# Kernel optimization log

Measured on AMD Instinct MI355X. Metric: run time of the kernel, lower is better.

Reference implementation:

```python
import jax, jax.numpy as jnp
import numpy as np

B, L, R, E, H = 256, 196, 1024, 1024, 512  # batch, regions, rnn_size, input_encoding, att_hid


def _lstm_cell(x, h, c, Wih, Whh, bih, bhh):
    # PyTorch LSTMCell gate order: i, f, g, o
    gates = x @ Wih.T + bih + h @ Whh.T + bhh  # [B, 4R]
    i, f, g, o = jnp.split(gates, 4, axis=1)
    i, f, o = jax.nn.sigmoid(i), jax.nn.sigmoid(f), jax.nn.sigmoid(o)
    g = jnp.tanh(g)
    c_new = f * c + i * g
    h_new = o * jnp.tanh(c_new)
    return h_new, c_new


def _attention(h, att_feats, p_att, mask, Wh, bh, Wa, ba):
    att_h = h @ Wh.T + bh                       # [B, H]
    dot = jnp.tanh(p_att + att_h[:, None, :])   # [B, L, H]
    scores = jnp.einsum('blh,h->bl', dot, Wa) + ba  # [B, L]
    w = jax.nn.softmax(scores, axis=1)
    w = w * mask
    w = w / (jnp.sum(w, axis=1, keepdims=True) + 1e-10)
    return jnp.einsum('bl,bld->bd', w, att_feats)  # [B, R]


def setup_inputs() -> dict:
    key = jax.random.key(0)
    ks = jax.random.split(key, 32)
    s = 0.05
    inp = {
        'xt': jax.random.normal(ks[0], (B, E), jnp.float32),
        'fc_feats': jax.random.normal(ks[1], (B, 3 * R), jnp.float32),
        'att_feats': jax.random.normal(ks[2], (B, L, R), jnp.float32),
        'p_att_feats': jax.random.normal(ks[3], (B, L, H), jnp.float32),
        'att_masks': jnp.ones((B, L), jnp.float32),
        'att_feats1': jax.random.normal(ks[4], (B, L, R), jnp.float32),
        'p_att_feats1': jax.random.normal(ks[5], (B, L, H), jnp.float32),
        'att_masks1': jnp.ones((B, L), jnp.float32),
        'state_h': jax.random.normal(ks[6], (3, B, R), jnp.float32),
        'state_c': jax.random.normal(ks[7], (3, B, R), jnp.float32),
        # att_lstm0 / att_lstm: input dim E + 2R; lang_lstm: 3R
        'Wih0': jax.random.normal(ks[8], (4 * R, E + 2 * R), jnp.float32) * s,
        'Whh0': jax.random.normal(ks[9], (4 * R, R), jnp.float32) * s,
        'bih0': jnp.zeros((4 * R,), jnp.float32),
        'bhh0': jnp.zeros((4 * R,), jnp.float32),
        'Wih1': jax.random.normal(ks[10], (4 * R, E + 2 * R), jnp.float32) * s,
        'Whh1': jax.random.normal(ks[11], (4 * R, R), jnp.float32) * s,
        'bih1': jnp.zeros((4 * R,), jnp.float32),
        'bhh1': jnp.zeros((4 * R,), jnp.float32),
        'WihL': jax.random.normal(ks[12], (4 * R, 3 * R), jnp.float32) * s,
        'WhhL': jax.random.normal(ks[13], (4 * R, R), jnp.float32) * s,
        'bihL': jnp.zeros((4 * R,), jnp.float32),
        'bhhL': jnp.zeros((4 * R,), jnp.float32),
        # attention0 / attention / attention1 params (h2att + alpha_net)
        'a0_Wh': jax.random.normal(ks[14], (H, R), jnp.float32) * s,
        'a0_bh': jnp.zeros((H,), jnp.float32),
        'a0_Wa': jax.random.normal(ks[15], (H,), jnp.float32) * s,
        'a0_ba': jnp.zeros((), jnp.float32),
        'a_Wh': jax.random.normal(ks[16], (H, R), jnp.float32) * s,
        'a_bh': jnp.zeros((H,), jnp.float32),
        'a_Wa': jax.random.normal(ks[17], (H,), jnp.float32) * s,
        'a_ba': jnp.zeros((), jnp.float32),
        'a1_Wh': jax.random.normal(ks[18], (H, R), jnp.float32) * s,
        'a1_bh': jnp.zeros((H,), jnp.float32),
        'a1_Wa': jax.random.normal(ks[19], (H,), jnp.float32) * s,
        'a1_ba': jnp.zeros((), jnp.float32),
    }
    return inp


def reference(xt, fc_feats, att_feats, p_att_feats, att_masks,
              att_feats1, p_att_feats1, att_masks1, state_h, state_c,
              Wih0, Whh0, bih0, bhh0, Wih1, Whh1, bih1, bhh1,
              WihL, WhhL, bihL, bhhL,
              a0_Wh, a0_bh, a0_Wa, a0_ba,
              a_Wh, a_bh, a_Wa, a_ba,
              a1_Wh, a1_bh, a1_Wa, a1_ba):
    prev_h = state_h[-1]                       # h_lang from previous step
    fc_ori = fc_feats[:, :R]                   # only the first slice is used

    # layer 0: att_lstm0 + attention0 over (att_feats1, p_att_feats1)
    x0 = jnp.concatenate([prev_h, fc_ori, xt], axis=1)
    h_att0, c_att0 = _lstm_cell(x0, state_h[0], state_c[0], Wih0, Whh0, bih0, bhh0)
    att0 = _attention(h_att0, att_feats1, p_att_feats1, att_masks1, a0_Wh, a0_bh, a0_Wa, a0_ba)

    # layer 1: att_lstm + two attentions
    x1 = jnp.concatenate([prev_h, att0, xt], axis=1)
    h_att, c_att = _lstm_cell(x1, state_h[1], state_c[1], Wih1, Whh1, bih1, bhh1)
    att = _attention(h_att, att_feats, p_att_feats, att_masks, a_Wh, a_bh, a_Wa, a_ba)
    att1 = _attention(h_att, att_feats1, p_att_feats1, att_masks1, a1_Wh, a1_bh, a1_Wa, a1_ba)

    # layer 2: lang_lstm
    xL = jnp.concatenate([att, att1, h_att], axis=1)
    h_lang, c_lang = _lstm_cell(xL, state_h[2], state_c[2], WihL, WhhL, bihL, bhhL)

    output = h_lang  # dropout is identity in eval mode
    new_h = jnp.stack([h_att0, h_att, h_lang])
    new_c = jnp.stack([c_att0, c_att, c_lang])
    return output, new_h, new_c
```

## Files before the change

kernel.cpp:

```cpp
#include <hip/hip_runtime.h>
#include <math.h>

#define B_   256
#define L_   196
#define R_   1024
#define E_   1024
#define H_   512
#define G4R  4096
#define DIN  3072

typedef short v4s __attribute__((ext_vector_type(4)));
typedef short v8s __attribute__((ext_vector_type(8)));
typedef float v4f __attribute__((ext_vector_type(4)));

__device__ __forceinline__ float sigmoidf_(float x) {
    return 1.0f / (1.0f + __expf(-x));
}
__device__ __forceinline__ float tanhf_(float x) {
    float ax = fabsf(x);
    float t  = __expf(-2.0f * ax);
    float r  = (1.0f - t) / (1.0f + t);
    return copysignf(r, x);
}

__device__ __forceinline__ void split2(float x, short& hi, short& lo) {
    unsigned u = __float_as_uint(x);
    hi = (short)(u >> 16);
    float r = x - __uint_as_float(u & 0xFFFF0000u);
    lo = (short)(__float_as_uint(r) >> 16);
}

template<int MT, int NT>
__global__ __launch_bounds__(256) void gemm_mfma(
    const float* __restrict__ A1, const float* __restrict__ W1, int K1, int lda1,
    const float* __restrict__ A2, const float* __restrict__ W2, int K2, int lda2,
    const float* __restrict__ bias1, const float* __restrict__ bias2,
    float* __restrict__ C, int N)
{
    constexpr int FM  = MT / 32;
    constexpr int FN  = NT / 32;
    constexpr int ACH = (MT * 32) / 1024;
    constexpr int WCH = (NT * 32) / 1024;

    __shared__ alignas(16) short Ahi[MT][40];
    __shared__ alignas(16) short Alo[MT][40];
    __shared__ alignas(16) short Whi[NT][40];
    __shared__ alignas(16) short Wlo[NT][40];

    const int t     = threadIdx.x;
    const int lane  = t & 63;
    const int wave  = t >> 6;
    const int waveM = wave & 1;
    const int waveN = wave >> 1;
    const int l16   = lane & 15;
    const int quad  = lane >> 4;
    const int mBase = blockIdx.x * MT;
    const int nBase = blockIdx.y * NT;

    v4f acc[FM][FN] = {};

    for (int seg = 0; seg < 2; ++seg) {
        const int K = seg ? K2 : K1;
        if (K == 0) continue;
        const float* Ag  = seg ? A2 : A1;
        const float* Wg  = seg ? W2 : W1;
        const int    lda = seg ? lda2 : lda1;

        for (int k0 = 0; k0 < K; k0 += 32) {
            __syncthreads();
            #pragma unroll
            for (int c = 0; c < ACH; ++c) {
                int flat = t * 4 + c * 1024;
                int row  = flat >> 5, k = flat & 31;
                float4 v = *(const float4*)(Ag + (size_t)(mBase + row) * lda + k0 + k);
                short h0, h1, h2, h3, l0, l1, l2, l3;
                split2(v.x, h0, l0); split2(v.y, h1, l1);
                split2(v.z, h2, l2); split2(v.w, h3, l3);
                v4s hv = { h0, h1, h2, h3 };
                v4s lv = { l0, l1, l2, l3 };
                *(v4s*)&Ahi[row][k] = hv;
                *(v4s*)&Alo[row][k] = lv;
            }
            #pragma unroll
            for (int c = 0; c < WCH; ++c) {
                int flat = t * 4 + c * 1024;
                int row  = flat >> 5, k = flat & 31;
                float4 v = *(const float4*)(Wg + (size_t)(nBase + row) * K + k0 + k);
                short h0, h1, h2, h3, l0, l1, l2, l3;
                split2(v.x, h0, l0); split2(v.y, h1, l1);
                split2(v.z, h2, l2); split2(v.w, h3, l3);
                v4s hv = { h0, h1, h2, h3 };
                v4s lv = { l0, l1, l2, l3 };
                *(v4s*)&Whi[row][k] = hv;
                *(v4s*)&Wlo[row][k] = lv;
            }
            __syncthreads();

            v8s ah[FM], al[FM], wh[FN], wl[FN];
            #pragma unroll
            for (int fi = 0; fi < FM; ++fi) {
                int r = waveM * (MT / 2) + fi * 16 + l16;
                ah[fi] = *(const v8s*)&Ahi[r][quad * 8];
                al[fi] = *(const v8s*)&Alo[r][quad * 8];
            }
            #pragma unroll
            for (int fj = 0; fj < FN; ++fj) {
                int r = waveN * (NT / 2) + fj * 16 + l16;
                wh[fj] = *(const v8s*)&Whi[r][quad * 8];
                wl[fj] = *(const v8s*)&Wlo[r][quad * 8];
            }

            #pragma unroll
            for (int fi = 0; fi < FM; ++fi)
                #pragma unroll
                for (int fj = 0; fj < FN; ++fj) {
                    acc[fi][fj] = __builtin_amdgcn_mfma_f32_16x16x32_bf16(
                        al[fi], wh[fj], acc[fi][fj], 0, 0, 0);
                    acc[fi][fj] = __builtin_amdgcn_mfma_f32_16x16x32_bf16(
                        ah[fi], wl[fj], acc[fi][fj], 0, 0, 0);
                    acc[fi][fj] = __builtin_amdgcn_mfma_f32_16x16x32_bf16(
                        ah[fi], wh[fj], acc[fi][fj], 0, 0, 0);
                }
        }
    }

    #pragma unroll
    for (int fj = 0; fj < FN; ++fj) {
        int n = nBase + waveN * (NT / 2) + fj * 16 + l16;
        float bb = bias1[n] + (bias2 ? bias2[n] : 0.0f);
        #pragma unroll
        for (int fi = 0; fi < FM; ++fi) {
            int m0 = mBase + waveM * (MT / 2) + fi * 16 + quad * 4;
            #pragma unroll
            for (int r = 0; r < 4; ++r)
                C[(size_t)(m0 + r) * N + n] = acc[fi][fj][r] + bb;
        }
    }
}

__global__ __launch_bounds__(256) void lstm_cell(
    const float* __restrict__ gates, const float* __restrict__ c_in,
    float* __restrict__ h_out, float* __restrict__ c_out,
    float* __restrict__ h_out2)
{
    int e = blockIdx.x * 256 + threadIdx.x;
    int b = e >> 10;
    int j = e & 1023;
    const float* g = gates + (size_t)b * G4R;
    float i_ = sigmoidf_(g[j]);
    float f_ = sigmoidf_(g[j + 1024]);
    float gg = tanhf_(g[j + 2048]);
    float o_ = sigmoidf_(g[j + 3072]);
    float c  = f_ * c_in[e] + i_ * gg;
    float h  = o_ * tanhf_(c);
    c_out[e] = c;
    h_out[e] = h;
    if (h_out2) h_out2[e] = h;
}

__global__ __launch_bounds__(256) void concat3_1024(
    float* __restrict__ dst,
    const float* __restrict__ s0, int ld0,
    const float* __restrict__ s1, int ld1,
    const float* __restrict__ s2, int ld2)
{
    int e = blockIdx.x * 256 + threadIdx.x;
    int b = e / 3072;
    int c = e - b * 3072;
    int which = c >> 10, off = c & 1023;
    const float* s = (which == 0) ? s0 : (which == 1) ? s1 : s2;
    int ld = (which == 0) ? ld0 : (which == 1) ? ld1 : ld2;
    dst[e] = s[(size_t)b * ld + off];
}

__global__ __launch_bounds__(64) void attn_scores(
    const float* __restrict__ p_att,
    const float* __restrict__ att_h,
    const float* __restrict__ Wa,
    const float* __restrict__ ba,
    float* __restrict__ scores)
{
    int l = blockIdx.x;
    int b = blockIdx.y;
    int lane = threadIdx.x;
    const float* p  = p_att + ((size_t)b * L_ + l) * H_;
    const float* ah = att_h + (size_t)b * H_;
    float sum = 0.0f;
#pragma unroll
    for (int i = 0; i < H_ / 64; i++) {
        int h = lane + i * 64;
        sum += tanhf_(p[h] + ah[h]) * Wa[h];
    }
    for (int off = 32; off; off >>= 1) sum += __shfl_down(sum, off);
    if (lane == 0) scores[(size_t)b * L_ + l] = sum + ba[0];
}

__global__ __launch_bounds__(256) void attn_softmax(
    const float* __restrict__ scores, const float* __restrict__ mask,
    float* __restrict__ w)
{
    int b = blockIdx.x;
    int t = threadIdx.x;
    __shared__ float red[256];
    float v = (t < L_) ? scores[(size_t)b * L_ + t] : -1e30f;
    red[t] = v; __syncthreads();
    for (int s = 128; s; s >>= 1) {
        if (t < s) red[t] = fmaxf(red[t], red[t + s]);
        __syncthreads();
    }
    float mx = red[0]; __syncthreads();
    float e = (t < L_) ? __expf(v - mx) : 0.0f;
    red[t] = e; __syncthreads();
    for (int s = 128; s; s >>= 1) {
        if (t < s) red[t] += red[t + s];
        __syncthreads();
    }
    float denom = red[0]; __syncthreads();
    float wm = (t < L_) ? (e / denom) * mask[(size_t)b * L_ + t] : 0.0f;
    red[t] = wm; __syncthreads();
    for (int s = 128; s; s >>= 1) {
        if (t < s) red[t] += red[t + s];
        __syncthreads();
    }
    float denom2 = red[0] + 1e-10f;
    if (t < L_) w[(size_t)b * L_ + t] = wm / denom2;
}

__global__ __launch_bounds__(256) void attn_wsum(
    const float* __restrict__ w,
    const float* __restrict__ feats,
    float* __restrict__ out)
{
    int b = blockIdx.y;
    int r = blockIdx.x * 256 + threadIdx.x;
    __shared__ float ws[L_];
    for (int i = threadIdx.x; i < L_; i += 256)
        ws[i] = w[(size_t)b * L_ + i];
    __syncthreads();
    const float* f = feats + (size_t)b * L_ * R_ + r;
    float a0 = 0, a1 = 0, a2 = 0, a3 = 0;
    for (int l = 0; l < L_; l += 4) {
        a0 += ws[l + 0] * f[(size_t)(l + 0) * R_];
        a1 += ws[l + 1] * f[(size_t)(l + 1) * R_];
        a2 += ws[l + 2] * f[(size_t)(l + 2) * R_];
        a3 += ws[l + 3] * f[(size_t)(l + 3) * R_];
    }
    out[(size_t)b * R_ + r] = a0 + a1 + a2 + a3;
}

extern "C" void kernel_launch(void* const* d_in, const int* in_sizes, int n_in,
                              void* d_out, int out_size, void* d_ws, size_t ws_size,
                              hipStream_t stream)
{
    const float* xt         = (const float*)d_in[0];
    const float* fc_feats   = (const float*)d_in[1];
    const float* att_feats  = (const float*)d_in[2];
    const float* p_att      = (const float*)d_in[3];
    const float* mask       = (const float*)d_in[4];
    const float* att_feats1 = (const float*)d_in[5];
    const float* p_att1     = (const float*)d_in[6];
    const float* mask1      = (const float*)d_in[7];
    const float* state_h    = (const float*)d_in[8];
    const float* state_c    = (const float*)d_in[9];
    const float* Wih0 = (const float*)d_in[10];
    const float* Whh0 = (const float*)d_in[11];
    const float* bih0 = (const float*)d_in[12];
    const float* bhh0 = (const float*)d_in[13];
    const float* Wih1 = (const float*)d_in[14];
    const float* Whh1 = (const float*)d_in[15];
    const float* bih1 = (const float*)d_in[16];
    const float* bhh1 = (const float*)d_in[17];
    const float* WihL = (const float*)d_in[18];
    const float* WhhL = (const float*)d_in[19];
    const float* bihL = (const float*)d_in[20];
    const float* bhhL = (const float*)d_in[21];
    const float* a0_Wh = (const float*)d_in[22];
    const float* a0_bh = (const float*)d_in[23];
    const float* a0_Wa = (const float*)d_in[24];
    const float* a0_ba = (const float*)d_in[25];
    const float* a_Wh  = (const float*)d_in[26];
    const float* a_bh  = (const float*)d_in[27];
    const float* a_Wa  = (const float*)d_in[28];
    const float* a_ba  = (const float*)d_in[29];
    const float* a1_Wh = (const float*)d_in[30];
    const float* a1_bh = (const float*)d_in[31];
    const float* a1_Wa = (const float*)d_in[32];
    const float* a1_ba = (const float*)d_in[33];

    const size_t BR = (size_t)B_ * R_;
    float* out   = (float*)d_out;
    float* h0    = out + 1 * BR;
    float* h1    = out + 2 * BR;
    float* h2    = out + 3 * BR;
    float* c0    = out + 4 * BR;
    float* c1    = out + 5 * BR;
    float* c2    = out + 6 * BR;

    float* xbuf  = (float*)d_ws;
    float* gates = xbuf + (size_t)B_ * DIN;
    float* atth  = gates + (size_t)B_ * G4R;
    float* sc    = atth + (size_t)B_ * H_;
    float* att0  = sc + (size_t)B_ * L_;
    float* attA  = att0 + BR;
    float* attB  = attA + BR;

    const float* prev_h = state_h + 2 * BR;

    dim3 gG(B_ / 64, G4R / 64);
    dim3 gA(B_ / 32, H_ / 32);
    dim3 gS(L_, B_);
    dim3 gW(R_ / 256, B_);

    concat3_1024<<<(B_ * DIN) / 256, 256, 0, stream>>>(xbuf, prev_h, R_, fc_feats, 3 * R_, xt, E_);
    gemm_mfma<64, 64><<<gG, 256, 0, stream>>>(xbuf, Wih0, DIN, DIN,
                                              state_h, Whh0, R_, R_,
                                              bih0, bhh0, gates, G4R);
    lstm_cell<<<(B_ * R_) / 256, 256, 0, stream>>>(gates, state_c, h0, c0, nullptr);

    gemm_mfma<32, 32><<<gA, 256, 0, stream>>>(h0, a0_Wh, R_, R_,
                                              nullptr, nullptr, 0, 0,
                                              a0_bh, nullptr, atth, H_);
    attn_scores<<<gS, 64, 0, stream>>>(p_att1, atth, a0_Wa, a0_ba, sc);
    attn_softmax<<<B_, 256, 0, stream>>>(sc, mask1, sc);
    attn_wsum<<<gW, 256, 0, stream>>>(sc, att_feats1, att0);

    concat3_1024<<<(B_ * DIN) / 256, 256, 0, stream>>>(xbuf, prev_h, R_, att0, R_, xt, E_);
    gemm_mfma<64, 64><<<gG, 256, 0, stream>>>(xbuf, Wih1, DIN, DIN,
                                              state_h + BR, Whh1, R_, R_,
                                              bih1, bhh1, gates, G4R);
    lstm_cell<<<(B_ * R_) / 256, 256, 0, stream>>>(gates, state_c + BR, h1, c1, nullptr);

    gemm_mfma<32, 32><<<gA, 256, 0, stream>>>(h1, a_Wh, R_, R_,
                                              nullptr, nullptr, 0, 0,
                                              a_bh, nullptr, atth, H_);
    attn_scores<<<gS, 64, 0, stream>>>(p_att, atth, a_Wa, a_ba, sc);
    attn_softmax<<<B_, 256, 0, stream>>>(sc, mask, sc);
    attn_wsum<<<gW, 256, 0, stream>>>(sc, att_feats, attA);

    gemm_mfma<32, 32><<<gA, 256, 0, stream>>>(h1, a1_Wh, R_, R_,
                                              nullptr, nullptr, 0, 0,
                                              a1_bh, nullptr, atth, H_);
    attn_scores<<<gS, 64, 0, stream>>>(p_att1, atth, a1_Wa, a1_ba, sc);
    attn_softmax<<<B_, 256, 0, stream>>>(sc, mask1, sc);
    attn_wsum<<<gW, 256, 0, stream>>>(sc, att_feats1, attB);

    concat3_1024<<<(B_ * DIN) / 256, 256, 0, stream>>>(xbuf, attA, R_, attB, R_, h1, R_);
    gemm_mfma<64, 64><<<gG, 256, 0, stream>>>(xbuf, WihL, DIN, DIN,
                                              state_h + 2 * BR, WhhL, R_, R_,
                                              bihL, bhhL, gates, G4R);
    lstm_cell<<<(B_ * R_) / 256, 256, 0, stream>>>(gates, state_c + 2 * BR, h2, c2, out);
}
```

Before: 1.215 ms.

## Replace concat+LSTM GEMM with multi-source pipelined bf16x3 MFMA GEMM

Adds a gemm_big kernel that reads the three concatenated input slices and the recurrent state straight from their source pointers, which removes the three concat3 kernels and their xbuf round trip. The kernel double-buffers LDS with register prefetch, uses 16x16x32 bf16 MFMA with a hi/lo split to keep fp32-like accuracy, and swizzles block IDs across a 1D grid of 256 blocks. It is hardcoded to K=4096 in 64-wide steps and the fixed problem shape, which trades generality for fewer launches and better load overlap.

```diff
diff --git a/kernel.cpp b/kernel.cpp
--- a/kernel.cpp
+++ b/kernel.cpp
@@ -28,6 +28,133 @@
     hi = (short)(u >> 16);
     float r = x - __uint_as_float(u & 0xFFFF0000u);
     lo = (short)(__float_as_uint(r) >> 16);
+}
+
+__global__ __launch_bounds__(256) void gemm_big(
+    const float* __restrict__ a0, int lda0,
+    const float* __restrict__ a1, int lda1,
+    const float* __restrict__ a2, int lda2,
+    const float* __restrict__ a3, int lda3,
+    const float* __restrict__ w0, int ldw0,
+    const float* __restrict__ w1, int ldw1,
+    const float* __restrict__ w2, int ldw2,
+    const float* __restrict__ w3, int ldw3,
+    const float* __restrict__ bias1, const float* __restrict__ bias2,
+    float* __restrict__ C)
+{
+    __shared__ alignas(16) short lds[2][4][64][72];
+
+    const int t     = threadIdx.x;
+    const int lane  = t & 63;
+    const int wave  = t >> 6;
+    const int waveM = wave & 1;
+    const int waveN = wave >> 1;
+    const int l16   = lane & 15;
+    const int quad  = lane >> 4;
+
+    const int bid = blockIdx.x;
+    const int wg  = ((bid & 7) << 5) | (bid >> 3);
+    const int mBase = (wg & 3) * 64;
+    const int nBase = (wg >> 2) * 64;
+
+    const int rowA = t >> 4;
+    const int kkA  = (t & 15) * 4;
+
+    v4f acc[2][2] = {};
+
+    auto loadT = [&](int i, float4* RA, float4* RW) {
+        const int s  = i >> 4;
+        const int k0 = (i & 15) << 6;
+        const float* pa = (s == 0) ? a0 : (s == 1) ? a1 : (s == 2) ? a2 : a3;
+        const int    la = (s == 0) ? lda0 : (s == 1) ? lda1 : (s == 2) ? lda2 : lda3;
+        const float* pw = (s == 0) ? w0 : (s == 1) ? w1 : (s == 2) ? w2 : w3;
+        const int    lw = (s == 0) ? ldw0 : (s == 1) ? ldw1 : (s == 2) ? ldw2 : ldw3;
+        pa += (size_t)mBase * la + k0 + kkA;
+        pw += (size_t)nBase * lw + k0 + kkA;
+#pragma unroll
+        for (int c = 0; c < 4; ++c) {
+            RA[c] = *(const float4*)(pa + (size_t)(rowA + c * 16) * la);
+            RW[c] = *(const float4*)(pw + (size_t)(rowA + c * 16) * lw);
+        }
+    };
+
+    auto storeT = [&](int buf, const float4* RA, const float4* RW) {
+#pragma unroll
+        for (int c = 0; c < 4; ++c) {
+            const int row = rowA + c * 16;
+            short h0, h1, h2, h3, l0, l1, l2, l3;
+            split2(RA[c].x, h0, l0); split2(RA[c].y, h1, l1);
+            split2(RA[c].z, h2, l2); split2(RA[c].w, h3, l3);
+            v4s hv = { h0, h1, h2, h3 };
+            v4s lv = { l0, l1, l2, l3 };
+            *(v4s*)&lds[buf][0][row][kkA] = hv;
+            *(v4s*)&lds[buf][1][row][kkA] = lv;
+            split2(RW[c].x, h0, l0); split2(RW[c].y, h1, l1);
+            split2(RW[c].z, h2, l2); split2(RW[c].w, h3, l3);
+            v4s hw = { h0, h1, h2, h3 };
+            v4s lw = { l0, l1, l2, l3 };
+            *(v4s*)&lds[buf][2][row][kkA] = hw;
+            *(v4s*)&lds[buf][3][row][kkA] = lw;
+        }
+    };
+
+    auto compT = [&](int buf) {
+#pragma unroll
+        for (int s = 0; s < 2; ++s) {
+            v8s ah[2], al[2], wh[2], wl[2];
+#pragma unroll
+            for (int fi = 0; fi < 2; ++fi) {
+                int r = waveM * 32 + fi * 16 + l16;
+                ah[fi] = *(const v8s*)&lds[buf][0][r][s * 32 + quad * 8];
+                al[fi] = *(const v8s*)&lds[buf][1][r][s * 32 + quad * 8];
+            }
+#pragma unroll
+            for (int fj = 0; fj < 2; ++fj) {
+                int r = waveN * 32 + fj * 16 + l16;
+                wh[fj] = *(const v8s*)&lds[buf][2][r][s * 32 + quad * 8];
+                wl[fj] = *(const v8s*)&lds[buf][3][r][s * 32 + quad * 8];
+            }
+#pragma unroll
+            for (int fi = 0; fi < 2; ++fi)
+#pragma unroll
+                for (int fj = 0; fj < 2; ++fj) {
+                    acc[fi][fj] = __builtin_amdgcn_mfma_f32_16x16x32_bf16(
+                        al[fi], wh[fj], acc[fi][fj], 0, 0, 0);
+                    acc[fi][fj] = __builtin_amdgcn_mfma_f32_16x16x32_bf16(
+                        ah[fi], wl[fj], acc[fi][fj], 0, 0, 0);
+                    acc[fi][fj] = __builtin_amdgcn_mfma_f32_16x16x32_bf16(
+                        ah[fi], wh[fj], acc[fi][fj], 0, 0, 0);
+                }
+        }
+    };
+
+    float4 rA0[4], rW0[4], rA1[4], rW1[4];
+    loadT(0, rA0, rW0);
+
+#pragma unroll 1
+    for (int i = 0; i < 64; i += 2) {
+        storeT(0, rA0, rW0);
+        loadT(i + 1, rA1, rW1);
+        __syncthreads();
+        compT(0);
+        storeT(1, rA1, rW1);
+        if (i + 2 < 64) loadT(i + 2, rA0, rW0);
+        __syncthreads();
+        compT(1);
+    }
+
+#pragma unroll
+    for (int fj = 0; fj < 2; ++fj) {
+        int n = nBase + waveN * 32 + fj * 16 + l16;
+        float bb = bias1[n] + bias2[n];
+#pragma unroll
+        for (int fi = 0; fi < 2; ++fi) {
+            int m0 = mBase + waveM * 32 + fi * 16 + quad * 4;
+#pragma unroll
+            for (int r = 0; r < 4; ++r)
+                C[(size_t)(m0 + r) * G4R + n] = acc[fi][fj][r] + bb;
+        }
+    }
 }
 
 template<int MT, int NT>
@@ -156,21 +283,6 @@
     c_out[e] = c;
     h_out[e] = h;
     if (h_out2) h_out2[e] = h;
-}
-
-__global__ __launch_bounds__(256) void concat3_1024(
-    float* __restrict__ dst,
-    const float* __restrict__ s0, int ld0,
-    const float* __restrict__ s1, int ld1,
-    const float* __restrict__ s2, int ld2)
-{
-    int e = blockIdx.x * 256 + threadIdx.x;
-    int b = e / 3072;
-    int c = e - b * 3072;
-    int which = c >> 10, off = c & 1023;
-    const float* s = (which == 0) ? s0 : (which == 1) ? s1 : s2;
-    int ld = (which == 0) ? ld0 : (which == 1) ? ld1 : ld2;
-    dst[e] = s[(size_t)b * ld + off];
 }
 
 __global__ __launch_bounds__(64) void attn_scores(
@@ -306,15 +418,14 @@
 
     const float* prev_h = state_h + 2 * BR;
 
-    dim3 gG(B_ / 64, G4R / 64);
     dim3 gA(B_ / 32, H_ / 32);
     dim3 gS(L_, B_);
     dim3 gW(R_ / 256, B_);
 
-    concat3_1024<<<(B_ * DIN) / 256, 256, 0, stream>>>(xbuf, prev_h, R_, fc_feats, 3 * R_, xt, E_);
-    gemm_mfma<64, 64><<<gG, 256, 0, stream>>>(xbuf, Wih0, DIN, DIN,
-                                              state_h, Whh0, R_, R_,
-                                              bih0, bhh0, gates, G4R);
+    gemm_big<<<256, 256, 0, stream>>>(
+        prev_h, R_, fc_feats, 3 * R_, xt, E_, state_h, R_,
+        Wih0, DIN, Wih0 + 1024, DIN, Wih0 + 2048, DIN, Whh0, R_,
+        bih0, bhh0, gates);
     lstm_cell<<<(B_ * R_) / 256, 256, 0, stream>>>(gates, state_c, h0, c0, nullptr);
 
     gemm_mfma<32, 32><<<gA, 256, 0, stream>>>(h0, a0_Wh, R_, R_,
@@ -324,10 +435,10 @@
     attn_softmax<<<B_, 256, 0, stream>>>(sc, mask1, sc);
     attn_wsum<<<gW, 256, 0, stream>>>(sc, att_feats1, att0);
 
-    concat3_1024<<<(B_ * DIN) / 256, 256, 0, stream>>>(xbuf, prev_h, R_, att0, R_, xt, E_);
-    gemm_mfma<64, 64><<<gG, 256, 0, stream>>>(xbuf, Wih1, DIN, DIN,
-                                              state_h + BR, Whh1, R_, R_,
-                                              bih1, bhh1, gates, G4R);
+    gemm_big<<<256, 256, 0, stream>>>(
+        prev_h, R_, att0, R_, xt, E_, state_h + BR, R_,
+        Wih1, DIN, Wih1 + 1024, DIN, Wih1 + 2048, DIN, Whh1, R_,
+        bih1, bhh1, gates);
     lstm_cell<<<(B_ * R_) / 256, 256, 0, stream>>>(gates, state_c + BR, h1, c1, nullptr);
 
     gemm_mfma<32, 32><<<gA, 256, 0, stream>>>(h1, a_Wh, R_, R_,
@@ -344,9 +455,9 @@
     attn_softmax<<<B_, 256, 0, stream>>>(sc, mask1, sc);
     attn_wsum<<<gW, 256, 0, stream>>>(sc, att_feats1, attB);
 
-    concat3_1024<<<(B_ * DIN) / 256, 256, 0, stream>>>(xbuf, attA, R_, attB, R_, h1, R_);
-    gemm_mfma<64, 64><<<gG, 256, 0, stream>>>(xbuf, WihL, DIN, DIN,
-                                              state_h + 2 * BR, WhhL, R_, R_,
-                                              bihL, bhhL, gates, G4R);
+    gemm_big<<<256, 256, 0, stream>>>(
+        attA, R_, attB, R_, h1, R_, state_h + 2 * BR, R_,
+        WihL, DIN, WihL + 1024, DIN, WihL + 2048, DIN, WhhL, R_,
+        bihL, bhhL, gates);
     lstm_cell<<<(B_ * R_) / 256, 256, 0, stream>>>(gates, state_c + 2 * BR, h2, c2, out);
 }
```

After: 1.171 ms. 1.04x faster.
